# Kernel tuning notes

Hardware: AMD Instinct MI355X
Metric: run time of the kernel (lower is better)

Reference implementation:

```python
import jax, jax.numpy as jnp
import numpy as np

B, S_ENC, S_DEC, ENC_H, DEC_H = 8, 2048, 2048, 512, 512


def setup_inputs() -> dict:
    key = jax.random.key(0)
    k1, k2, k3 = jax.random.split(key, 3)
    return {
        "enc_hidden_states": jax.random.normal(k1, (B, S_ENC, ENC_H), dtype=jnp.float32),
        "dec_hidden_states": jax.random.normal(k2, (B, S_DEC, DEC_H), dtype=jnp.float32),
        "W_att": jax.random.normal(k3, (ENC_H, DEC_H), dtype=jnp.float32),
    }


def reference(enc_hidden_states, dec_hidden_states, W_att):
    # Project encoder states: [B, S_enc, dec_h]
    enc_proj = jnp.einsum("bse,ed->bsd", enc_hidden_states, W_att)
    # Luong 'general' scores for all decoder timesteps at once: [B, S_dec, S_enc]
    # (original code loops over decoder timesteps via tf.map_fn; this is the
    # equivalent single batched matmul)
    att_logits = jnp.einsum("btd,bsd->bts", dec_hidden_states, enc_proj)
    att_softmax = jax.nn.softmax(att_logits, axis=-1)
    # Attention context vectors: [B, S_dec, enc_h]
    att_vector = jnp.einsum("bts,bse->bte", att_softmax, enc_hidden_states)
    return att_vector
```

## Files before the change

### kernel.cpp

```cpp
#include <hip/hip_runtime.h>
#include <cstdint>


#define DEVINL __device__ __forceinline__

typedef __attribute__((ext_vector_type(8))) short short8;
typedef __attribute__((ext_vector_type(4))) short short4v;
typedef __attribute__((ext_vector_type(4))) float f32x4;

DEVINL short f2bf(float x) {
    union { float f; uint32_t u; } v; v.f = x;
    uint32_t r = v.u + 0x7FFFu + ((v.u >> 16) & 1u);
    return (short)(r >> 16);
}
DEVINL float bf2f(short h) {
    union { uint32_t u; float f; } v; v.u = ((uint32_t)(uint16_t)h) << 16;
    return v.f;
}

DEVINL void gload_lds16(const void* g, void* l) {
    __builtin_amdgcn_global_load_lds(
        (const __attribute__((address_space(1))) char*)g,
        (__attribute__((address_space(3))) char*)l, 16, 0, 0);
}

__global__ __launch_bounds__(256)
void split_kernel(const float* __restrict__ x, short* __restrict__ hi,
                  short* __restrict__ lo)
{
    long i = ((long)blockIdx.x * 256 + threadIdx.x) * 8;
    f32x4 a = *(const f32x4*)(x + i);
    f32x4 b = *(const f32x4*)(x + i + 4);
    short8 h, l;
#pragma unroll
    for (int j = 0; j < 4; j++) {
        short ha = f2bf(a[j]); h[j] = ha;     l[j] = f2bf(a[j] - bf2f(ha));
        short hb = f2bf(b[j]); h[4 + j] = hb; l[4 + j] = f2bf(b[j] - bf2f(hb));
    }
    *(short8*)(hi + i) = h;
    *(short8*)(lo + i) = l;
}

__global__ __launch_bounds__(256)
void split_w_kernel(const float* __restrict__ w, short* __restrict__ wth,
                    short* __restrict__ wtl)
{
    int idx = blockIdx.x * 256 + threadIdx.x;
    int k = idx >> 9, n = idx & 511;
    float v = w[idx];
    short h = f2bf(v);
    wth[(long)n * 512 + k] = h;
    wtl[(long)n * 512 + k] = f2bf(v - bf2f(h));
}

__global__ __launch_bounds__(256)
void transpose_bf16_kernel(const short* __restrict__ x, short* __restrict__ xt)
{
    __shared__ short tile[32][33];
    const int b  = blockIdx.z;
    const int s0 = blockIdx.x * 32;
    const int e0 = blockIdx.y * 32;
    const short* px = x + (long)b * 2048 * 512;
    short* pt = xt + (long)b * 512 * 2048;
    const int tx = threadIdx.x & 31;
    const int ty = threadIdx.x >> 5;
#pragma unroll
    for (int r = 0; r < 32; r += 8)
        tile[ty + r][tx] = px[(long)(s0 + ty + r) * 512 + e0 + tx];
    __syncthreads();
#pragma unroll
    for (int r = 0; r < 32; r += 8)
        pt[(long)(e0 + ty + r) * 2048 + s0 + tx] = tile[tx][ty + r];
}

template<int NTERMS, bool SPLIT_OUT, bool STATS>
__global__ __launch_bounds__(256, 2)
void gemm_bt(const short* __restrict__ Ah, const short* __restrict__ Al,
             const short* __restrict__ Bh, const short* __restrict__ Bl,
             float* __restrict__ C, short* __restrict__ Ch, short* __restrict__ Cl,
             float2* __restrict__ stats,
             int K, int lda, int ldb, int ldc,
             long sA, long sB, long sC)
{
    extern __shared__ char smem_raw[];
    constexpr int OPS = (NTERMS == 3) ? 4 : 2;
    constexpr int SET = 128 * 32 * OPS;
    short* smem = (short*)smem_raw;

    const int tid  = threadIdx.x;
    const int wave = tid >> 6;
    const int lane = tid & 63;
    const int quad = lane >> 4;
    const int l16  = lane & 15;
    const int wm   = (wave >> 1) * 64;
    const int wn   = (wave & 1) * 64;

    const long tile_m = (long)blockIdx.y * 128;
    const long tile_n = (long)blockIdx.x * 128;
    const int  bz     = blockIdx.z;

    const short* pAh = Ah + (long)bz * sA;
    const short* pBh = Bh + (long)bz * sB;
    const short* pAl = (NTERMS == 3) ? (Al + (long)bz * sA) : nullptr;
    const short* pBl = (NTERMS == 3) ? (Bl + (long)bz * sB) : nullptr;

    const int srow = tid >> 2;
    const int skq  = (tid & 3) * 8;
    const int lds_off = srow * 32 + skq;
    const long ga0 = (tile_m + srow) * (long)lda + skq;
    const long gb0 = (tile_n + srow) * (long)ldb + skq;

    auto stage = [&](int k0, int buf) {
        short* s   = smem + buf * SET;
        short* ash = s;
        short* bsh = s + 128 * 32;
        gload_lds16(pAh + ga0 + k0,             ash + lds_off);
        gload_lds16(pAh + ga0 + 64l * lda + k0, ash + lds_off + 64 * 32);
        gload_lds16(pBh + gb0 + k0,             bsh + lds_off);
        gload_lds16(pBh + gb0 + 64l * ldb + k0, bsh + lds_off + 64 * 32);
        if constexpr (NTERMS == 3) {
            short* asl = s + 2 * 128 * 32;
            short* bsl = s + 3 * 128 * 32;
            gload_lds16(pAl + ga0 + k0,             asl + lds_off);
            gload_lds16(pAl + ga0 + 64l * lda + k0, asl + lds_off + 64 * 32);
            gload_lds16(pBl + gb0 + k0,             bsl + lds_off);
            gload_lds16(pBl + gb0 + 64l * ldb + k0, bsl + lds_off + 64 * 32);
        }
    };

    f32x4 acc[4][4] = {};
    stage(0, 0);
    int cur = 0;

    for (int k0 = 0; k0 < K; k0 += 32) {
        __syncthreads();
        if (k0 + 32 < K) stage(k0 + 32, cur ^ 1);

        short* s   = smem + cur * SET;
        short* ash = s;
        short* bsh = s + 128 * 32;
        short* asl = s + 2 * 128 * 32;
        short* bsl = s + 3 * 128 * 32;

        short8 ah[4], bh[4], al[4], bl[4];
#pragma unroll
        for (int i = 0; i < 4; i++) {
            ah[i] = *(const short8*)&ash[(wm + i * 16 + l16) * 32 + quad * 8];
            bh[i] = *(const short8*)&bsh[(wn + i * 16 + l16) * 32 + quad * 8];
            if constexpr (NTERMS == 3) {
                al[i] = *(const short8*)&asl[(wm + i * 16 + l16) * 32 + quad * 8];
                bl[i] = *(const short8*)&bsl[(wn + i * 16 + l16) * 32 + quad * 8];
            }
        }
#pragma unroll
        for (int i = 0; i < 4; i++)
#pragma unroll
            for (int j = 0; j < 4; j++) {
                acc[i][j] = __builtin_amdgcn_mfma_f32_16x16x32_bf16(ah[i], bh[j], acc[i][j], 0, 0, 0);
                if constexpr (NTERMS == 3) {
                    acc[i][j] = __builtin_amdgcn_mfma_f32_16x16x32_bf16(ah[i], bl[j], acc[i][j], 0, 0, 0);
                    acc[i][j] = __builtin_amdgcn_mfma_f32_16x16x32_bf16(al[i], bh[j], acc[i][j], 0, 0, 0);
                }
            }
        cur ^= 1;
    }

    if constexpr (STATS) {
        float* sred = (float*)(smem + 2 * SET);
        float mrow[4][4], lrow[4][4];
#pragma unroll
        for (int i = 0; i < 4; i++)
#pragma unroll
            for (int r = 0; r < 4; r++) {
                float m = acc[i][0][r];
#pragma unroll
                for (int j = 1; j < 4; j++) m = fmaxf(m, acc[i][j][r]);
                m = fmaxf(m, __shfl_xor(m, 1));
                m = fmaxf(m, __shfl_xor(m, 2));
                m = fmaxf(m, __shfl_xor(m, 4));
                m = fmaxf(m, __shfl_xor(m, 8));
                mrow[i][r] = m;
            }
        __syncthreads();
        if (l16 == 0) {
#pragma unroll
            for (int i = 0; i < 4; i++)
#pragma unroll
                for (int r = 0; r < 4; r++)
                    sred[(wm + i * 16 + quad * 4 + r) * 2 + (wave & 1)] = mrow[i][r];
        }
        __syncthreads();
#pragma unroll
        for (int i = 0; i < 4; i++)
#pragma unroll
            for (int r = 0; r < 4; r++) {
                int row = wm + i * 16 + quad * 4 + r;
                mrow[i][r] = fmaxf(sred[row * 2], sred[row * 2 + 1]);
            }
        __syncthreads();
#pragma unroll
        for (int i = 0; i < 4; i++)
#pragma unroll
            for (int r = 0; r < 4; r++) {
                float s = 0.f;
#pragma unroll
                for (int j = 0; j < 4; j++) s += __expf(acc[i][j][r] - mrow[i][r]);
                s += __shfl_xor(s, 1);
                s += __shfl_xor(s, 2);
                s += __shfl_xor(s, 4);
                s += __shfl_xor(s, 8);
                lrow[i][r] = s;
            }
        if (l16 == 0) {
#pragma unroll
            for (int i = 0; i < 4; i++)
#pragma unroll
                for (int r = 0; r < 4; r++)
                    sred[(wm + i * 16 + quad * 4 + r) * 2 + (wave & 1)] = lrow[i][r];
        }
        __syncthreads();
        if ((wave & 1) == 0 && l16 == 0) {
#pragma unroll
            for (int i = 0; i < 4; i++)
#pragma unroll
                for (int r = 0; r < 4; r++) {
                    int row = wm + i * 16 + quad * 4 + r;
                    long grow = tile_m + row;
                    float2 v; v.x = mrow[i][r];
                    v.y = sred[row * 2] + sred[row * 2 + 1];
                    stats[((long)bz * 2048 + grow) * 16 + blockIdx.x] = v;
                }
        }
    }

#pragma unroll
    for (int i = 0; i < 4; i++)
#pragma unroll
        for (int j = 0; j < 4; j++) {
            const long row0 = tile_m + wm + i * 16 + quad * 4;
            const long col  = tile_n + wn + j * 16 + l16;
#pragma unroll
            for (int r = 0; r < 4; r++) {
                float v = acc[i][j][r];
                if constexpr (SPLIT_OUT) {
                    long idx = (long)bz * sC + (row0 + r) * (long)ldc + col;
                    short h = f2bf(v);
                    Ch[idx] = h;
                    Cl[idx] = f2bf(v - bf2f(h));
                } else {
                    C[(long)bz * sC + (row0 + r) * (long)ldc + col] = v;
                }
            }
        }
}

__global__ __launch_bounds__(256)
void combine_kernel(const float2* __restrict__ stats, float* __restrict__ Mrow,
                    float* __restrict__ Linv)
{
    long r = (long)blockIdx.x * 256 + threadIdx.x;
    const float2* s = stats + r * 16;
    float2 v[16];
#pragma unroll
    for (int i = 0; i < 16; i++) v[i] = s[i];
    float m = v[0].x;
#pragma unroll
    for (int i = 1; i < 16; i++) m = fmaxf(m, v[i].x);
    float l = 0.f;
#pragma unroll
    for (int i = 0; i < 16; i++) l += v[i].y * __expf(v[i].x - m);
    Mrow[r] = m;
    Linv[r] = 1.f / l;
}

__global__ __launch_bounds__(512, 2)
void pv_wide(const float* __restrict__ S, const short* __restrict__ encT,
             const float* __restrict__ Mrow, const float* __restrict__ Linv,
             float* __restrict__ Out)
{
    extern __shared__ char smem_raw[];
    short* As = (short*)smem_raw;

    const int tid  = threadIdx.x;
    const int wave = tid >> 6;
    const int lane = tid & 63;
    const int quad = lane >> 4;
    const int l16  = lane & 15;

    const int  bz     = blockIdx.y;
    const long tile_m = (long)blockIdx.x * 64;

    const int arow  = tid >> 3;
    const int acol  = (tid & 7) * 4;
    const float* pS = S + ((long)bz * 2048 + tile_m + arow) * 2048 + acol;
    const int aoff  = arow * 32 + acol;
    const float m_r = Mrow[bz * 2048 + tile_m + arow];

    const short* pB = encT + (long)bz * 512 * 2048
                    + (long)(wave * 64 + l16) * 2048 + quad * 8;

    f32x4 acc[4][4] = {};
    short8 bfr[2][4];
    f32x4 sp[2];

    {
        f32x4 s0 = *(const f32x4*)pS;
        short4v h;
#pragma unroll
        for (int e = 0; e < 4; e++) h[e] = f2bf(__expf(s0[e] - m_r));
        *(short4v*)(As + aoff) = h;
    }
    sp[1] = *(const f32x4*)(pS + 32);
#pragma unroll
    for (int j = 0; j < 4; j++)
        bfr[0][j] = *(const short8*)(pB + (long)j * 16 * 2048);

    auto step = [&](int k0, int p) {
        __syncthreads();
        const bool more  = (k0 + 32 < 2048);
        const bool more2 = (k0 + 64 < 2048);
        if (more2) sp[p] = *(const f32x4*)(pS + k0 + 64);
        if (more) {
#pragma unroll
            for (int j = 0; j < 4; j++)
                bfr[p ^ 1][j] = *(const short8*)(pB + (long)j * 16 * 2048 + k0 + 32);
        }
        short8 a[4];
#pragma unroll
        for (int i = 0; i < 4; i++)
            a[i] = *(const short8*)&As[p * 2048 + (i * 16 + l16) * 32 + quad * 8];
#pragma unroll
        for (int i = 0; i < 4; i++)
#pragma unroll
            for (int j = 0; j < 4; j++)
                acc[i][j] = __builtin_amdgcn_mfma_f32_16x16x32_bf16(a[i], bfr[p][j], acc[i][j], 0, 0, 0);
        if (more) {
            f32x4 sv = sp[p ^ 1];
            short4v h;
#pragma unroll
            for (int e = 0; e < 4; e++) h[e] = f2bf(__expf(sv[e] - m_r));
            *(short4v*)(As + (p ^ 1) * 2048 + aoff) = h;
        }
    };

    for (int k0 = 0; k0 < 2048; k0 += 64) {
        step(k0, 0);
        step(k0 + 32, 1);
    }

    float li[4][4];
#pragma unroll
    for (int i = 0; i < 4; i++)
#pragma unroll
        for (int r = 0; r < 4; r++)
            li[i][r] = Linv[bz * 2048 + tile_m + i * 16 + quad * 4 + r];
#pragma unroll
    for (int i = 0; i < 4; i++)
#pragma unroll
        for (int j = 0; j < 4; j++) {
            const long row0 = tile_m + i * 16 + quad * 4;
            const long col  = wave * 64 + j * 16 + l16;
#pragma unroll
            for (int r = 0; r < 4; r++)
                Out[((long)bz * 2048 + row0 + r) * 512 + col] = acc[i][j][r] * li[i][r];
        }
}

extern "C" void kernel_launch(void* const* d_in, const int* in_sizes, int n_in,
                              void* d_out, int out_size, void* d_ws, size_t ws_size,
                              hipStream_t stream)
{
    const float* enc = (const float*)d_in[0];
    const float* dec = (const float*)d_in[1];
    const float* W   = (const float*)d_in[2];
    float* out = (float*)d_out;

    const long BSE = 8l * 2048 * 512;
    const long NW  = 512l * 512;

    char* p = (char*)d_ws;
    auto take = [&](long bytes) { char* r = p; p += (bytes + 255) & ~255l; return r; };
    short* enc_hi = (short*)take(BSE * 2);
    short* enc_lo = (short*)take(BSE * 2);
    short* dec_hi = (short*)take(BSE * 2);
    short* dec_lo = (short*)take(BSE * 2);
    short* ep_hi  = (short*)take(BSE * 2);
    short* ep_lo  = (short*)take(BSE * 2);
    short* enc_t  = (short*)take(BSE * 2);
    short* wt_hi  = (short*)take(NW * 2);
    short* wt_lo  = (short*)take(NW * 2);
    float* logits = (float*)take(8l * 2048 * 2048 * 4);
    float2* stats = (float2*)enc_lo;
    float*  MrowA = (float*)(enc_lo + 4l * 1024 * 1024);
    float*  LinvA = (float*)(enc_lo + 5l * 1024 * 1024);
    (void)ws_size; (void)in_sizes; (void)n_in; (void)out_size;

    split_kernel<<<4096, 256, 0, stream>>>(enc, enc_hi, enc_lo);
    split_kernel<<<4096, 256, 0, stream>>>(dec, dec_hi, dec_lo);
    split_w_kernel<<<1024, 256, 0, stream>>>(W, wt_hi, wt_lo);
    transpose_bf16_kernel<<<dim3(64, 16, 8), 256, 0, stream>>>(enc_hi, enc_t);

    gemm_bt<3, true, false><<<dim3(4, 128, 1), 256, 64 * 1024, stream>>>(
        enc_hi, enc_lo, wt_hi, wt_lo, nullptr, ep_hi, ep_lo, nullptr,
        512, 512, 512, 512, 0, 0, 0);

    gemm_bt<3, false, true><<<dim3(16, 16, 8), 256, 64 * 1024 + 1024, stream>>>(
        dec_hi, dec_lo, ep_hi, ep_lo, logits, nullptr, nullptr, stats,
        512, 512, 512, 2048, 2048l * 512, 2048l * 512, 2048l * 2048);

    combine_kernel<<<64, 256, 0, stream>>>(stats, MrowA, LinvA);

    pv_wide<<<dim3(32, 8), 512, 8 * 1024, stream>>>(
        logits, enc_t, MrowA, LinvA, out);
}
```

Before: 370.2 us.

## Fuse encoder split with transpose and use 32x32 MFMA for projection GEMM

Merges the encoder fp32-to-bf16 hi/lo split into the transpose kernel, so the encoder is read once and one launch is removed. It also replaces the projection GEMM with a new kernel that uses 32x32x16 bf16 MFMA instructions, a K-step of 16 and half the LDS, for higher MFMA throughput per LDS read and more blocks per CU. The fused kernel writes hi/lo with scalar 2-byte stores instead of vectorized ones. The new GEMM's K loop is short and double-buffered with a sync every step, which may limit overlap.

```diff
diff --git a/kernel.cpp b/kernel.cpp
--- a/kernel.cpp
+++ b/kernel.cpp
@@ -4,9 +4,10 @@
 
 #define DEVINL __device__ __forceinline__
 
-typedef __attribute__((ext_vector_type(8))) short short8;
-typedef __attribute__((ext_vector_type(4))) short short4v;
-typedef __attribute__((ext_vector_type(4))) float f32x4;
+typedef __attribute__((ext_vector_type(8)))  short short8;
+typedef __attribute__((ext_vector_type(4)))  short short4v;
+typedef __attribute__((ext_vector_type(4)))  float f32x4;
+typedef __attribute__((ext_vector_type(16))) float f32x16;
 
 DEVINL short f2bf(float x) {
     union { float f; uint32_t u; } v; v.f = x;
@@ -54,19 +55,25 @@
 }
 
 __global__ __launch_bounds__(256)
-void transpose_bf16_kernel(const short* __restrict__ x, short* __restrict__ xt)
+void encprep_kernel(const float* __restrict__ enc, short* __restrict__ hi,
+                    short* __restrict__ lo, short* __restrict__ xt)
 {
     __shared__ short tile[32][33];
     const int b  = blockIdx.z;
     const int s0 = blockIdx.x * 32;
     const int e0 = blockIdx.y * 32;
-    const short* px = x + (long)b * 2048 * 512;
     short* pt = xt + (long)b * 512 * 2048;
     const int tx = threadIdx.x & 31;
     const int ty = threadIdx.x >> 5;
 #pragma unroll
-    for (int r = 0; r < 32; r += 8)
-        tile[ty + r][tx] = px[(long)(s0 + ty + r) * 512 + e0 + tx];
+    for (int r = 0; r < 32; r += 8) {
+        long idx = (long)b * 2048 * 512 + (long)(s0 + ty + r) * 512 + e0 + tx;
+        float v = enc[idx];
+        short h = f2bf(v);
+        hi[idx] = h;
+        lo[idx] = f2bf(v - bf2f(h));
+        tile[ty + r][tx] = h;
+    }
     __syncthreads();
 #pragma unroll
     for (int r = 0; r < 32; r += 8)
@@ -250,6 +257,87 @@
                 } else {
                     C[(long)bz * sC + (row0 + r) * (long)ldc + col] = v;
                 }
+            }
+        }
+}
+
+__global__ __launch_bounds__(256, 2)
+void gemm_bt32_split(const short* __restrict__ Ah, const short* __restrict__ Al,
+                     const short* __restrict__ Bh, const short* __restrict__ Bl,
+                     short* __restrict__ Ch, short* __restrict__ Cl,
+                     int K, int lda, int ldb, int ldc)
+{
+    extern __shared__ char smem_raw[];
+    constexpr int PL  = 128 * 16;
+    constexpr int SET = PL * 4;
+    short* smem = (short*)smem_raw;
+
+    const int tid   = threadIdx.x;
+    const int wave  = tid >> 6;
+    const int lane  = tid & 63;
+    const int l32   = lane & 31;
+    const int khalf = lane >> 5;
+    const int wm    = (wave >> 1) * 64;
+    const int wn    = (wave & 1) * 64;
+
+    const long tile_m = (long)blockIdx.y * 128;
+    const long tile_n = (long)blockIdx.x * 128;
+
+    const int srow = tid >> 1;
+    const int skq  = (tid & 1) * 8;
+    const int lds_off = srow * 16 + skq;
+    const long ga0 = (tile_m + srow) * (long)lda + skq;
+    const long gb0 = (tile_n + srow) * (long)ldb + skq;
+
+    auto stage = [&](int k0, int buf) {
+        short* s = smem + buf * SET;
+        gload_lds16(Ah + ga0 + k0, s + lds_off);
+        gload_lds16(Bh + gb0 + k0, s + PL + lds_off);
+        gload_lds16(Al + ga0 + k0, s + 2 * PL + lds_off);
+        gload_lds16(Bl + gb0 + k0, s + 3 * PL + lds_off);
+    };
+
+    f32x16 acc[2][2] = {};
+    stage(0, 0);
+    int cur = 0;
+
+    for (int k0 = 0; k0 < K; k0 += 16) {
+        __syncthreads();
+        if (k0 + 16 < K) stage(k0 + 16, cur ^ 1);
+
+        short* s = smem + cur * SET;
+        short8 ah[2], bh[2], al[2], bl[2];
+#pragma unroll
+        for (int i = 0; i < 2; i++) {
+            ah[i] = *(const short8*)&s[(wm + i * 32 + l32) * 16 + khalf * 8];
+            bh[i] = *(const short8*)&s[PL + (wn + i * 32 + l32) * 16 + khalf * 8];
+            al[i] = *(const short8*)&s[2 * PL + (wm + i * 32 + l32) * 16 + khalf * 8];
+            bl[i] = *(const short8*)&s[3 * PL + (wn + i * 32 + l32) * 16 + khalf * 8];
+        }
+#pragma unroll
+        for (int i = 0; i < 2; i++)
+#pragma unroll
+            for (int j = 0; j < 2; j++) {
+                acc[i][j] = __builtin_amdgcn_mfma_f32_32x32x16_bf16(ah[i], bh[j], acc[i][j], 0, 0, 0);
+                acc[i][j] = __builtin_amdgcn_mfma_f32_32x32x16_bf16(ah[i], bl[j], acc[i][j], 0, 0, 0);
+                acc[i][j] = __builtin_amdgcn_mfma_f32_32x32x16_bf16(al[i], bh[j], acc[i][j], 0, 0, 0);
+            }
+        cur ^= 1;
+    }
+
+#pragma unroll
+    for (int i = 0; i < 2; i++)
+#pragma unroll
+        for (int j = 0; j < 2; j++) {
+            const long colg = tile_n + wn + j * 32 + l32;
+#pragma unroll
+            for (int r = 0; r < 16; r++) {
+                const long rowg = tile_m + wm + i * 32 + (r & 3) + 8 * (r >> 2) + 4 * khalf;
+                float v = acc[i][j][r];
+                long idx = rowg * (long)ldc + colg;
+                short h = f2bf(v);
+                Ch[idx] = h;
+                Cl[idx] = f2bf(v - bf2f(h));
             }
         }
 }
@@ -395,14 +483,13 @@
     float*  LinvA = (float*)(enc_lo + 5l * 1024 * 1024);
     (void)ws_size; (void)in_sizes; (void)n_in; (void)out_size;
 
-    split_kernel<<<4096, 256, 0, stream>>>(enc, enc_hi, enc_lo);
+    encprep_kernel<<<dim3(64, 16, 8), 256, 0, stream>>>(enc, enc_hi, enc_lo, enc_t);
     split_kernel<<<4096, 256, 0, stream>>>(dec, dec_hi, dec_lo);
     split_w_kernel<<<1024, 256, 0, stream>>>(W, wt_hi, wt_lo);
-    transpose_bf16_kernel<<<dim3(64, 16, 8), 256, 0, stream>>>(enc_hi, enc_t);
-
-    gemm_bt<3, true, false><<<dim3(4, 128, 1), 256, 64 * 1024, stream>>>(
-        enc_hi, enc_lo, wt_hi, wt_lo, nullptr, ep_hi, ep_lo, nullptr,
-        512, 512, 512, 512, 0, 0, 0);
+
+    gemm_bt32_split<<<dim3(4, 128, 1), 256, 32 * 1024, stream>>>(
+        enc_hi, enc_lo, wt_hi, wt_lo, ep_hi, ep_lo,
+        512, 512, 512, 512);
 
     gemm_bt<3, false, true><<<dim3(16, 16, 8), 256, 64 * 1024 + 1024, stream>>>(
         dec_hi, dec_lo, ep_hi, ep_lo, logits, nullptr, nullptr, stats,
```

Result: slower. 401.3 us (+8.4%).
